# Optimization experiments

Hardware: AMD Instinct MI355X
Metric: run time of the kernel (lower is better)

## Reference

```python
import jax, jax.numpy as jnp
import numpy as np

B, T, N = 2, 512, 512
H = 64          # hidden_dim
S = 8           # static_dim
C = 8           # coord_dim
DYN = 4         # dynamic feature dim (hard-coded in module)
SELF_LOOP_W = 1.0


def setup_inputs() -> dict:
    key = jax.random.key(0)
    ks = jax.random.split(key, 12)
    x = jax.random.normal(ks[0], (B, T, N), dtype=jnp.float32)
    mask = jax.random.randint(ks[1], (B, T, N), 0, 2).astype(jnp.float32)
    static_context = jax.random.normal(ks[2], (N, S), dtype=jnp.float32)
    node_coords = jax.random.normal(ks[3], (N, C), dtype=jnp.float32)
    sc = 0.1
    W1 = jax.random.normal(ks[4], (DYN + S, H), dtype=jnp.float32) * sc
    b1 = jnp.zeros((H,), dtype=jnp.float32)
    W2 = jax.random.normal(ks[5], (H, H), dtype=jnp.float32) * sc
    b2 = jnp.zeros((H,), dtype=jnp.float32)
    W3 = jax.random.normal(ks[6], (4 * H, H), dtype=jnp.float32) * sc
    b3 = jnp.zeros((H,), dtype=jnp.float32)
    W4 = jax.random.normal(ks[7], (H, 1), dtype=jnp.float32) * sc
    b4 = jnp.zeros((1,), dtype=jnp.float32)
    return {"x": x, "mask": mask, "static_context": static_context,
            "node_coords": node_coords, "W1": W1, "b1": b1, "W2": W2,
            "b2": b2, "W3": W3, "b3": b3, "W4": W4, "b4": b4}


def _dynamic_context(x, mask):
    observed = 1.0 - mask                                  # (B,T,N)
    count = jnp.maximum(observed.sum(axis=1), 1.0)          # (B,N)
    mean = (x * observed).sum(axis=1) / count               # (B,N)
    centered = (x - mean[:, None, :]) * observed
    std = jnp.sqrt((centered ** 2).sum(axis=1) / count + 1e-6)
    # last observed value per node
    t_idx = jnp.arange(x.shape[1], dtype=x.dtype)[None, :, None]
    latest = jnp.argmax(t_idx * observed, axis=1)           # (B,N) int
    last = jnp.take_along_axis(x, latest[:, None, :], axis=1)[:, 0, :]
    missing_ratio = mask.mean(axis=1)                       # (B,N)
    return jnp.stack([mean, std, last, missing_ratio], axis=-1)  # (B,N,4)


def _prior_adjacency(node_coords):
    diff = node_coords[:, None, :] - node_coords[None, :, :]  # (N,N,C)
    d2 = (diff ** 2).sum(-1)
    dist = jnp.where(d2 > 0, jnp.sqrt(jnp.where(d2 > 0, d2, 1.0)), 0.0)
    prior = 1.0 / (1.0 + dist)
    eye = jnp.eye(node_coords.shape[0], dtype=node_coords.dtype)
    return prior * (1.0 - eye)


def reference(x, mask, static_context, node_coords, W1, b1, W2, b2, W3, b3, W4, b4):
    batch = x.shape[0]
    node_dynamic = _dynamic_context(x, mask)                         # (B,N,4)
    node_static = jnp.broadcast_to(static_context[None], (batch,) + static_context.shape)
    feats = jnp.concatenate([node_dynamic, node_static], axis=-1)    # (B,N,4+S)
    h = jax.nn.relu(feats @ W1 + b1)
    node_repr = jax.nn.relu(h @ W2 + b2)                              # (B,N,H)

    h_i = node_repr[:, :, None, :]                                    # (B,N,1,H)
    h_j = node_repr[:, None, :, :]                                    # (B,1,N,H)
    hi = jnp.broadcast_to(h_i, (batch, N, N, H))
    hj = jnp.broadcast_to(h_j, (batch, N, N, H))
    pair = jnp.concatenate([hi, hj, jnp.abs(hi - hj), hi * hj], axis=-1)  # (B,N,N,4H)
    e = jax.nn.relu(pair @ W3 + b3)
    edge_mod = jax.nn.relu((e @ W4 + b4)[..., 0])                     # (B,N,N)

    prior = _prior_adjacency(node_coords)[None]                       # (1,N,N)
    eye = jnp.eye(N, dtype=x.dtype)[None]
    adapt = edge_mod * prior + eye * SELF_LOOP_W
    degree = jnp.maximum(adapt.sum(axis=-1), 1e-6)                    # (B,N)
    inv_sqrt = degree ** -0.5
    return inv_sqrt[:, :, None] * adapt * inv_sqrt[:, None, :]
```

## Files before the change

kernel.cpp:

```cpp
#include <hip/hip_runtime.h>
#include <math.h>

#define B_ 2
#define T_ 512
#define N_ 512
#define H_ 64

typedef _Float16 half8 __attribute__((ext_vector_type(8)));
typedef __attribute__((ext_vector_type(4))) float floatx4;

__device__ inline half8 habs8(half8 v) {
    union { half8 h; unsigned u[4]; } x; x.h = v;
    x.u[0] &= 0x7fff7fffu; x.u[1] &= 0x7fff7fffu;
    x.u[2] &= 0x7fff7fffu; x.u[3] &= 0x7fff7fffu;
    return x.h;
}

__global__ void prep_kernel(const float* __restrict__ x, const float* __restrict__ mask,
                            const float* __restrict__ coords, const float* __restrict__ W3,
                            float* __restrict__ part, float* __restrict__ prior,
                            _Float16* __restrict__ W3ph) {
    int blk = blockIdx.x;
    if (blk < 512) {
        int b  = blk >> 8;
        int nc = (blk >> 5) & 7;
        int tc = blk & 31;
        int tn = threadIdx.x & 63;
        int tt = threadIdx.x >> 6;
        int n  = nc * 64 + tn;

        float sx = 0.f, sxx = 0.f, cnt = 0.f, msum = 0.f, bv = 0.f, bt = -1.f;
#pragma unroll
        for (int it = 0; it < 4; it++) {
            int t = tc * 16 + it * 4 + tt;
            int off = (b * T_ + t) * N_ + n;
            float xv = x[off];
            float mv = mask[off];
            float obs = 1.f - mv;
            sx   += xv * obs;
            sxx  += xv * xv * obs;
            cnt  += obs;
            msum += mv;
            if (obs > 0.5f) { bt = (float)t; bv = xv; }
        }

        __shared__ float red[6][4][64];
        red[0][tt][tn] = sx;  red[1][tt][tn] = sxx; red[2][tt][tn] = cnt;
        red[3][tt][tn] = msum; red[4][tt][tn] = bv; red[5][tt][tn] = bt;
        __syncthreads();

        if (threadIdx.x < 64) {
            float Sx = 0.f, Sxx = 0.f, Cnt = 0.f, Ms = 0.f, Bv = 0.f, Bt = -1.f;
#pragma unroll
            for (int u = 0; u < 4; u++) {
                Sx  += red[0][u][tn];
                Sxx += red[1][u][tn];
                Cnt += red[2][u][tn];
                Ms  += red[3][u][tn];
                float btu = red[5][u][tn];
                if (btu > Bt) { Bt = btu; Bv = red[4][u][tn]; }
            }
            const int plane = B_ * 32 * N_;
            int base = (b * 32 + tc) * N_ + n;
            part[0 * plane + base] = Sx;
            part[1 * plane + base] = Sxx;
            part[2 * plane + base] = Cnt;
            part[3 * plane + base] = Ms;
            part[4 * plane + base] = Bv;
            part[5 * plane + base] = Bt;
        }
    } else if (blk < 1536) {
        int idx = (blk - 512) * 256 + threadIdx.x;
        int i = idx >> 9, j = idx & (N_ - 1);
        float d2 = 0.f;
#pragma unroll
        for (int c = 0; c < 8; c++) {
            float df = coords[i * 8 + c] - coords[j * 8 + c];
            d2 += df * df;
        }
        float dist = (d2 > 0.f) ? sqrtf(d2) : 0.f;
        prior[idx] = (i == j) ? 0.f : 1.f / (1.f + dist);
    } else {
        int k = (blk - 1536) * 256 + threadIdx.x;
        int t = k & 7;
        int l = (k >> 3) & 63;
        int f = k >> 9;
        int s = f >> 2, nt = f & 3;
        int quad = l >> 4, col = l & 15;
        W3ph[k] = (_Float16)W3[(128 + s * 32 + quad * 8 + t) * H_ + nt * 16 + col];
    }
}

__global__ __launch_bounds__(64) void node_kernel(
        const float* __restrict__ part, const float* __restrict__ x,
        const float* __restrict__ sc,
        const float* __restrict__ W1, const float* __restrict__ b1,
        const float* __restrict__ W2, const float* __restrict__ b2,
        const float* __restrict__ W3,
        _Float16* __restrict__ nrh, float* __restrict__ P, float* __restrict__ Qp) {
    int blk = blockIdx.x;
    int b = blk >> 9;
    int n = blk & (N_ - 1);
    int o = threadIdx.x;

    __shared__ float f[12];
    __shared__ float h[H_];
    __shared__ float r[H_];

    {
        const int plane = B_ * 32 * N_;
        float Sx = 0.f, Sxx = 0.f, Cnt = 0.f, Ms = 0.f, Bv = 0.f, Bt = -1.f;
        if (o < 32) {
            int base = (b * 32 + o) * N_ + n;
            Sx  = part[0 * plane + base];
            Sxx = part[1 * plane + base];
            Cnt = part[2 * plane + base];
            Ms  = part[3 * plane + base];
            Bv  = part[4 * plane + base];
            Bt  = part[5 * plane + base];
        }
#pragma unroll
        for (int off = 1; off < 32; off <<= 1) {
            Sx  += __shfl_xor(Sx, off);
            Sxx += __shfl_xor(Sxx, off);
            Cnt += __shfl_xor(Cnt, off);
            Ms  += __shfl_xor(Ms, off);
            float obt = __shfl_xor(Bt, off);
            float obv = __shfl_xor(Bv, off);
            if (obt > Bt) { Bt = obt; Bv = obv; }
        }
        if (o == 0) {
            float count = fmaxf(Cnt, 1.f);
            float mean  = Sx / count;
            float var   = (Sxx - 2.f * mean * Sx + mean * mean * Cnt) / count;
            float stdv  = sqrtf(fmaxf(var, 0.f) + 1e-6f);
            float last  = (Bt >= 0.f) ? Bv : x[b * T_ * N_ + n];
            f[0] = mean; f[1] = stdv; f[2] = last; f[3] = Ms * (1.f / (float)T_);
        }
        if (o >= 4 && o < 12) f[o] = sc[n * 8 + (o - 4)];
    }
    __syncthreads();

    float a = b1[o];
#pragma unroll
    for (int k = 0; k < 12; k++) a += f[k] * W1[k * H_ + o];
    h[o] = fmaxf(a, 0.f);
    __syncthreads();

    float a2 = b2[o];
#pragma unroll 8
    for (int k = 0; k < H_; k++) a2 += h[k] * W2[k * H_ + o];
    float rv = fmaxf(a2, 0.f);
    r[o] = rv;
    nrh[(b * N_ + n) * H_ + o] = (_Float16)rv;
    __syncthreads();

    float p = 0.f, q = 0.f;
#pragma unroll 8
    for (int k = 0; k < H_; k++) {
        float rk = r[k];
        p += rk * W3[k * H_ + o];
        q += rk * W3[(H_ + k) * H_ + o];
    }
    P[(b * N_ + n) * H_ + o] = p;
    Qp[(b * N_ + n) * H_ + (o & 15) * 4 + (o >> 4)] = q;
}

__global__ __launch_bounds__(256) void pair_mfma_kernel(
        const _Float16* __restrict__ nrh, const float* __restrict__ P,
        const float* __restrict__ Qp, const _Float16* __restrict__ W3ph,
        const float* __restrict__ b3, const float* __restrict__ W4,
        const float* __restrict__ b4, const float* __restrict__ prior,
        float* __restrict__ adapt, float* __restrict__ degree) {
    int blk = blockIdx.x;
    int rb = blk >> 9;
    int i = blk & (N_ - 1);
    int tid = threadIdx.x;
    int w = tid >> 6;
    int l = tid & 63;
    int col = l & 15;
    int quad = l >> 4;

    half8 bf[4][4];
#pragma unroll
    for (int s = 0; s < 4; s++)
#pragma unroll
        for (int nt = 0; nt < 4; nt++)
            bf[s][nt] = *(const half8*)(W3ph + (((s * 4 + nt) * 64 + l) << 3));

    const _Float16* hi_row = nrh + (rb * N_ + i) * H_;
    half8 hiA = *(const half8*)(hi_row + quad * 8);
    half8 hiB = *(const half8*)(hi_row + 32 + quad * 8);

    float pb3[4], w4v[4];
#pragma unroll
    for (int nt = 0; nt < 4; nt++) {
        int o = nt * 16 + col;
        pb3[nt] = P[(rb * N_ + i) * H_ + o] + b3[o];
        w4v[nt] = W4[o];
    }
    float b4s = b4[0];
    const float* prow = prior + i * N_;
    const _Float16* nrb = nrh + (rb * N_) * H_;
    float rsum = 0.f;

    half8 hA, hB;
    {
        const _Float16* p0 = nrb + (w * 128 + col) * H_;
        hA = *(const half8*)(p0 + quad * 8);
        hB = *(const half8*)(p0 + 32 + quad * 8);
    }

#pragma unroll
    for (int mt = 0; mt < 8; mt++) {
        int j0 = w * 128 + mt * 16;

        half8 nA, nB;
        if (mt < 7) {
            const _Float16* pn = nrb + (j0 + 16 + col) * H_;
            nA = *(const half8*)(pn + quad * 8);
            nB = *(const half8*)(pn + 32 + quad * 8);
        }

        floatx4 pv = *(const floatx4*)(prow + j0 + quad * 4);
        floatx4 qv[4];
#pragma unroll
        for (int r = 0; r < 4; r++)
            qv[r] = *(const floatx4*)(Qp + (rb * N_ + j0 + quad * 4 + r) * H_ + col * 4);

        half8 dA = habs8(hiA - hA);
        half8 dB = habs8(hiB - hB);
        half8 mA = hiA * hA;
        half8 mB = hiB * hB;

        floatx4 acc[4];
#pragma unroll
        for (int nt = 0; nt < 4; nt++) acc[nt] = (floatx4){0.f, 0.f, 0.f, 0.f};
#pragma unroll
        for (int nt = 0; nt < 4; nt++) {
            acc[nt] = __builtin_amdgcn_mfma_f32_16x16x32_f16(dA, bf[0][nt], acc[nt], 0, 0, 0);
            acc[nt] = __builtin_amdgcn_mfma_f32_16x16x32_f16(dB, bf[1][nt], acc[nt], 0, 0, 0);
            acc[nt] = __builtin_amdgcn_mfma_f32_16x16x32_f16(mA, bf[2][nt], acc[nt], 0, 0, 0);
            acc[nt] = __builtin_amdgcn_mfma_f32_16x16x32_f16(mB, bf[3][nt], acc[nt], 0, 0, 0);
        }

        float ed[4];
#pragma unroll
        for (int r = 0; r < 4; r++) {
            int j = j0 + quad * 4 + r;
            float p = 0.f;
#pragma unroll
            for (int nt = 0; nt < 4; nt++)
                p += fmaxf(acc[nt][r] + pb3[nt] + qv[r][nt], 0.f) * w4v[nt];
            p += __shfl_xor(p, 1);
            p += __shfl_xor(p, 2);
            p += __shfl_xor(p, 4);
            p += __shfl_xor(p, 8);
            float edge = fmaxf(p + b4s, 0.f);
            float ad = (j == i) ? 1.0f : edge * pv[r];
            ed[r] = ad;
            rsum += ad;
        }
        if (col == 0) {
            *(floatx4*)&adapt[(size_t)(rb * N_ + i) * N_ + j0 + quad * 4] =
                (floatx4){ed[0], ed[1], ed[2], ed[3]};
        }
        if (mt < 7) { hA = nA; hB = nB; }
    }

    rsum += __shfl_xor(rsum, 16);
    rsum += __shfl_xor(rsum, 32);
    __shared__ float sRow[4];
    if (l == 0) sRow[w] = rsum;
    __syncthreads();
    if (tid == 0) degree[rb * N_ + i] = sRow[0] + sRow[1] + sRow[2] + sRow[3];
}

__global__ void norm_kernel(const float* __restrict__ adapt, const float* __restrict__ deg,
                            float* __restrict__ out) {
    int idx = blockIdx.x * 256 + threadIdx.x;
    int b = idx >> 16;
    int r = (idx >> 7) & (N_ - 1);
    int c4 = (idx & 127) << 2;
    float dr = rsqrtf(fmaxf(deg[b * N_ + r], 1e-6f));
    floatx4 a = *(const floatx4*)(adapt + ((size_t)idx << 2));
    floatx4 o;
#pragma unroll
    for (int k = 0; k < 4; k++)
        o[k] = dr * a[k] * rsqrtf(fmaxf(deg[b * N_ + c4 + k], 1e-6f));
    *(floatx4*)(out + ((size_t)idx << 2)) = o;
}

extern "C" void kernel_launch(void* const* d_in, const int* in_sizes, int n_in,
                              void* d_out, int out_size, void* d_ws, size_t ws_size,
                              hipStream_t stream) {
    const float* x      = (const float*)d_in[0];
    const float* mask   = (const float*)d_in[1];
    const float* sc     = (const float*)d_in[2];
    const float* coords = (const float*)d_in[3];
    const float* W1 = (const float*)d_in[4];
    const float* b1 = (const float*)d_in[5];
    const float* W2 = (const float*)d_in[6];
    const float* b2 = (const float*)d_in[7];
    const float* W3 = (const float*)d_in[8];
    const float* b3 = (const float*)d_in[9];
    const float* W4 = (const float*)d_in[10];
    const float* b4 = (const float*)d_in[11];
    float* out = (float*)d_out;

    float* wsp = (float*)d_ws;
    float* P       = wsp;
    float* Qp      = wsp + 65536;
    float* prior   = wsp + 131072;
    _Float16* nrh  = (_Float16*)(wsp + 393216);
    _Float16* W3ph = (_Float16*)(wsp + 425984);
    float* deg     = wsp + 430080;
    float* adapt   = wsp + 431104;
    float* part    = adapt;

    prep_kernel<<<1568, 256, 0, stream>>>(x, mask, coords, W3, part, prior, W3ph);
    node_kernel<<<B_ * N_, 64, 0, stream>>>(part, x, sc, W1, b1, W2, b2, W3, nrh, P, Qp);
    pair_mfma_kernel<<<B_ * N_, 256, 0, stream>>>(nrh, P, Qp, W3ph, b3, W4, b4, prior, adapt, deg);
    norm_kernel<<<512, 256, 0, stream>>>(adapt, deg, out);
}
```

Before: 110.7 us.

## Compute prior adjacency inside pair kernel and loop both batches per block

Removes the separate prior-matrix stage from the prep kernel. Each pair-kernel block now computes its row of prior distances into shared memory, and the block loops over both batch entries for the same row i. This avoids writing and re-reading the 1 MB prior matrix and reuses the W3 fragments and prior row across batches. The cost is half as many blocks, 512 instead of 1024, which reduces parallelism and latency hiding on a large GPU.

```diff
diff --git a/kernel.cpp b/kernel.cpp
--- a/kernel.cpp
+++ b/kernel.cpp
@@ -17,9 +17,8 @@
 }
 
 __global__ void prep_kernel(const float* __restrict__ x, const float* __restrict__ mask,
-                            const float* __restrict__ coords, const float* __restrict__ W3,
-                            float* __restrict__ part, float* __restrict__ prior,
-                            _Float16* __restrict__ W3ph) {
+                            const float* __restrict__ W3,
+                            float* __restrict__ part, _Float16* __restrict__ W3ph) {
     int blk = blockIdx.x;
     if (blk < 512) {
         int b  = blk >> 8;
@@ -69,19 +68,8 @@
             part[4 * plane + base] = Bv;
             part[5 * plane + base] = Bt;
         }
-    } else if (blk < 1536) {
-        int idx = (blk - 512) * 256 + threadIdx.x;
-        int i = idx >> 9, j = idx & (N_ - 1);
-        float d2 = 0.f;
-#pragma unroll
-        for (int c = 0; c < 8; c++) {
-            float df = coords[i * 8 + c] - coords[j * 8 + c];
-            d2 += df * df;
-        }
-        float dist = (d2 > 0.f) ? sqrtf(d2) : 0.f;
-        prior[idx] = (i == j) ? 0.f : 1.f / (1.f + dist);
     } else {
-        int k = (blk - 1536) * 256 + threadIdx.x;
+        int k = (blk - 512) * 256 + threadIdx.x;
         int t = k & 7;
         int l = (k >> 3) & 63;
         int f = k >> 9;
@@ -169,18 +157,36 @@
 __global__ __launch_bounds__(256) void pair_mfma_kernel(
         const _Float16* __restrict__ nrh, const float* __restrict__ P,
         const float* __restrict__ Qp, const _Float16* __restrict__ W3ph,
+        const float* __restrict__ coords,
         const float* __restrict__ b3, const float* __restrict__ W4,
-        const float* __restrict__ b4, const float* __restrict__ prior,
+        const float* __restrict__ b4,
         float* __restrict__ adapt, float* __restrict__ degree) {
-    int blk = blockIdx.x;
-    int rb = blk >> 9;
-    int i = blk & (N_ - 1);
+    int i = blockIdx.x;
     int tid = threadIdx.x;
     int w = tid >> 6;
     int l = tid & 63;
     int col = l & 15;
     int quad = l >> 4;
 
+    __shared__ float sPrior[N_];
+    __shared__ float sRow[B_][4];
+
+    {
+        float ci[8];
+#pragma unroll
+        for (int c = 0; c < 8; c++) ci[c] = coords[i * 8 + c];
+        for (int jj = tid; jj < N_; jj += 256) {
+            float d2 = 0.f;
+#pragma unroll
+            for (int c = 0; c < 8; c++) {
+                float df = ci[c] - coords[jj * 8 + c];
+                d2 += df * df;
+            }
+            float dist = (d2 > 0.f) ? sqrtf(d2) : 0.f;
+            sPrior[jj] = (jj == i) ? 0.f : 1.f / (1.f + dist);
+        }
+    }
+
     half8 bf[4][4];
 #pragma unroll
     for (int s = 0; s < 4; s++)
@@ -188,92 +194,102 @@
         for (int nt = 0; nt < 4; nt++)
             bf[s][nt] = *(const half8*)(W3ph + (((s * 4 + nt) * 64 + l) << 3));
 
-    const _Float16* hi_row = nrh + (rb * N_ + i) * H_;
-    half8 hiA = *(const half8*)(hi_row + quad * 8);
-    half8 hiB = *(const half8*)(hi_row + 32 + quad * 8);
-
-    float pb3[4], w4v[4];
+    float b3v[4], w4v[4];
 #pragma unroll
     for (int nt = 0; nt < 4; nt++) {
         int o = nt * 16 + col;
-        pb3[nt] = P[(rb * N_ + i) * H_ + o] + b3[o];
+        b3v[nt] = b3[o];
         w4v[nt] = W4[o];
     }
     float b4s = b4[0];
-    const float* prow = prior + i * N_;
-    const _Float16* nrb = nrh + (rb * N_) * H_;
-    float rsum = 0.f;
-
-    half8 hA, hB;
-    {
-        const _Float16* p0 = nrb + (w * 128 + col) * H_;
-        hA = *(const half8*)(p0 + quad * 8);
-        hB = *(const half8*)(p0 + 32 + quad * 8);
-    }
-
-#pragma unroll
-    for (int mt = 0; mt < 8; mt++) {
-        int j0 = w * 128 + mt * 16;
-
-        half8 nA, nB;
-        if (mt < 7) {
-            const _Float16* pn = nrb + (j0 + 16 + col) * H_;
-            nA = *(const half8*)(pn + quad * 8);
-            nB = *(const half8*)(pn + 32 + quad * 8);
-        }
-
-        floatx4 pv = *(const floatx4*)(prow + j0 + quad * 4);
-        floatx4 qv[4];
-#pragma unroll
-        for (int r = 0; r < 4; r++)
-            qv[r] = *(const floatx4*)(Qp + (rb * N_ + j0 + quad * 4 + r) * H_ + col * 4);
-
-        half8 dA = habs8(hiA - hA);
-        half8 dB = habs8(hiB - hB);
-        half8 mA = hiA * hA;
-        half8 mB = hiB * hB;
-
-        floatx4 acc[4];
-#pragma unroll
-        for (int nt = 0; nt < 4; nt++) acc[nt] = (floatx4){0.f, 0.f, 0.f, 0.f};
-#pragma unroll
-        for (int nt = 0; nt < 4; nt++) {
-            acc[nt] = __builtin_amdgcn_mfma_f32_16x16x32_f16(dA, bf[0][nt], acc[nt], 0, 0, 0);
-            acc[nt] = __builtin_amdgcn_mfma_f32_16x16x32_f16(dB, bf[1][nt], acc[nt], 0, 0, 0);
-            acc[nt] = __builtin_amdgcn_mfma_f32_16x16x32_f16(mA, bf[2][nt], acc[nt], 0, 0, 0);
-            acc[nt] = __builtin_amdgcn_mfma_f32_16x16x32_f16(mB, bf[3][nt], acc[nt], 0, 0, 0);
-        }
-
-        float ed[4];
-#pragma unroll
-        for (int r = 0; r < 4; r++) {
-            int j = j0 + quad * 4 + r;
-            float p = 0.f;
-#pragma unroll
-            for (int nt = 0; nt < 4; nt++)
-                p += fmaxf(acc[nt][r] + pb3[nt] + qv[r][nt], 0.f) * w4v[nt];
-            p += __shfl_xor(p, 1);
-            p += __shfl_xor(p, 2);
-            p += __shfl_xor(p, 4);
-            p += __shfl_xor(p, 8);
-            float edge = fmaxf(p + b4s, 0.f);
-            float ad = (j == i) ? 1.0f : edge * pv[r];
-            ed[r] = ad;
-            rsum += ad;
-        }
-        if (col == 0) {
-            *(floatx4*)&adapt[(size_t)(rb * N_ + i) * N_ + j0 + quad * 4] =
-                (floatx4){ed[0], ed[1], ed[2], ed[3]};
-        }
-        if (mt < 7) { hA = nA; hB = nB; }
-    }
-
-    rsum += __shfl_xor(rsum, 16);
-    rsum += __shfl_xor(rsum, 32);
-    __shared__ float sRow[4];
-    if (l == 0) sRow[w] = rsum;
-    __syncthreads();
-    if (tid == 0) degree[rb * N_ + i] = sRow[0] + sRow[1] + sRow[2] + sRow[3];
+    __syncthreads();
+
+#pragma unroll 1
+    for (int rb = 0; rb < B_; rb++) {
+        const _Float16* hi_row = nrh + (rb * N_ + i) * H_;
+        half8 hiA = *(const half8*)(hi_row + quad * 8);
+        half8 hiB = *(const half8*)(hi_row + 32 + quad * 8);
+
+        float pb3[4];
+#pragma unroll
+        for (int nt = 0; nt < 4; nt++)
+            pb3[nt] = P[(rb * N_ + i) * H_ + nt * 16 + col] + b3v[nt];
+
+        const _Float16* nrb = nrh + (rb * N_) * H_;
+        float rsum = 0.f;
+
+        half8 hA, hB;
+        {
+            const _Float16* p0 = nrb + (w * 128 + col) * H_;
+            hA = *(const half8*)(p0 + quad * 8);
+            hB = *(const half8*)(p0 + 32 + quad * 8);
+        }
+
+#pragma unroll
+        for (int mt = 0; mt < 8; mt++) {
+            int j0 = w * 128 + mt * 16;
+
+            half8 nA, nB;
+            if (mt < 7) {
+                const _Float16* pn = nrb + (j0 + 16 + col) * H_;
+                nA = *(const half8*)(pn + quad * 8);
+                nB = *(const half8*)(pn + 32 + quad * 8);
+            }
+
+            floatx4 pv = *(const floatx4*)(sPrior + j0 + quad * 4);
+            floatx4 qv[4];
+#pragma unroll
+            for (int r = 0; r < 4; r++)
+                qv[r] = *(const floatx4*)(Qp + (rb * N_ + j0 + quad * 4 + r) * H_ + col * 4);
+
+            half8 dA = habs8(hiA - hA);
+            half8 dB = habs8(hiB - hB);
+            half8 mA = hiA * hA;
+            half8 mB = hiB * hB;
+
+            floatx4 acc[4];
+#pragma unroll
+            for (int nt = 0; nt < 4; nt++) acc[nt] = (floatx4){0.f, 0.f, 0.f, 0.f};
+#pragma unroll
+            for (int nt = 0; nt < 4; nt++) {
+                acc[nt] = __builtin_amdgcn_mfma_f32_16x16x32_f16(dA, bf[0][nt], acc[nt], 0, 0, 0);
+                acc[nt] = __builtin_amdgcn_mfma_f32_16x16x32_f16(dB, bf[1][nt], acc[nt], 0, 0, 0);
+                acc[nt] = __builtin_amdgcn_mfma_f32_16x16x32_f16(mA, bf[2][nt], acc[nt], 0, 0, 0);
+                acc[nt] = __builtin_amdgcn_mfma_f32_16x16x32_f16(mB, bf[3][nt], acc[nt], 0, 0, 0);
+            }
+
+            float ed[4];
+#pragma unroll
+            for (int r = 0; r < 4; r++) {
+                int j = j0 + quad * 4 + r;
+                float p = 0.f;
+#pragma unroll
+                for (int nt = 0; nt < 4; nt++)
+                    p += fmaxf(acc[nt][r] + pb3[nt] + qv[r][nt], 0.f) * w4v[nt];
+                p += __shfl_xor(p, 1);
+                p += __shfl_xor(p, 2);
+                p += __shfl_xor(p, 4);
+                p += __shfl_xor(p, 8);
+                float edge = fmaxf(p + b4s, 0.f);
+                float ad = (j == i) ? 1.0f : edge * pv[r];
+                ed[r] = ad;
+                rsum += ad;
+            }
+            if (col == 0) {
+                *(floatx4*)&adapt[(size_t)(rb * N_ + i) * N_ + j0 + quad * 4] =
+                    (floatx4){ed[0], ed[1], ed[2], ed[3]};
+            }
+            if (mt < 7) { hA = nA; hB = nB; }
+        }
+
+        rsum += __shfl_xor(rsum, 16);
+        rsum += __shfl_xor(rsum, 32);
+        if (l == 0) sRow[rb][w] = rsum;
+    }
+
+    __syncthreads();
+    if (tid < B_)
+        degree[tid * N_ + i] = sRow[tid][0] + sRow[tid][1] + sRow[tid][2] + sRow[tid][3];
 }
 
 __global__ void norm_kernel(const float* __restrict__ adapt, const float* __restrict__ deg,
@@ -311,15 +327,14 @@
     float* wsp = (float*)d_ws;
     float* P       = wsp;
     float* Qp      = wsp + 65536;
-    float* prior   = wsp + 131072;
-    _Float16* nrh  = (_Float16*)(wsp + 393216);
-    _Float16* W3ph = (_Float16*)(wsp + 425984);
-    float* deg     = wsp + 430080;
-    float* adapt   = wsp + 431104;
+    _Float16* nrh  = (_Float16*)(wsp + 131072);
+    _Float16* W3ph = (_Float16*)(wsp + 163840);
+    float* deg     = wsp + 167936;
+    float* adapt   = wsp + 168960;
     float* part    = adapt;
 
-    prep_kernel<<<1568, 256, 0, stream>>>(x, mask, coords, W3, part, prior, W3ph);
+    prep_kernel<<<544, 256, 0, stream>>>(x, mask, W3, part, W3ph);
     node_kernel<<<B_ * N_, 64, 0, stream>>>(part, x, sc, W1, b1, W2, b2, W3, nrh, P, Qp);
-    pair_mfma_kernel<<<B_ * N_, 256, 0, stream>>>(nrh, P, Qp, W3ph, b3, W4, b4, prior, adapt, deg);
+    pair_mfma_kernel<<<N_, 256, 0, stream>>>(nrh, P, Qp, W3ph, coords, b3, W4, b4, adapt, deg);
     norm_kernel<<<512, 256, 0, stream>>>(adapt, deg, out);
 }
```

New measurement: 109.6 us. About the same (-1.0%).
